# Kernel optimization log

Measured on AMD Instinct MI355X. Metric: run time of the kernel, lower is better.

## Reference

```python
import jax, jax.numpy as jnp
import numpy as np

N_NODES = 8192
N_EDGES = 262144
IN_DIM = 256
HID = 256
OUT_DIM = 64
PATH_DIM = 64
N_HEADS = 4


def setup_inputs() -> dict:
    key = jax.random.key(0)
    ks = jax.random.split(key, 16)
    s = 0.05
    x = jax.random.normal(ks[0], (N_NODES, IN_DIM), dtype=jnp.float32)
    edge_index = jax.random.randint(ks[1], (2, N_EDGES), 0, N_NODES, dtype=jnp.int32)
    return {
        "x": x,
        "edge_index": edge_index,
        # pathway encoder Linear(IN_DIM, PATH_DIM)
        "pe_w": jax.random.normal(ks[2], (IN_DIM, PATH_DIM), jnp.float32) * s,
        "pe_b": jax.random.normal(ks[3], (PATH_DIM,), jnp.float32) * s,
        # MultiheadAttention packed in-proj [3E, E] and out-proj [E, E]
        "in_proj_w": jax.random.normal(ks[4], (3 * PATH_DIM, PATH_DIM), jnp.float32) * s,
        "in_proj_b": jax.random.normal(ks[5], (3 * PATH_DIM,), jnp.float32) * s,
        "out_proj_w": jax.random.normal(ks[6], (PATH_DIM, PATH_DIM), jnp.float32) * s,
        "out_proj_b": jax.random.normal(ks[7], (PATH_DIM,), jnp.float32) * s,
        # GCN layer weights (in_dim, out_dim) + bias
        "w1": jax.random.normal(ks[8], (IN_DIM + PATH_DIM, HID), jnp.float32) * s,
        "b1": jax.random.normal(ks[9], (HID,), jnp.float32) * s,
        "w2": jax.random.normal(ks[10], (HID, HID), jnp.float32) * s,
        "b2": jax.random.normal(ks[11], (HID,), jnp.float32) * s,
        "w3": jax.random.normal(ks[12], (HID, OUT_DIM), jnp.float32) * s,
        "b3": jax.random.normal(ks[13], (OUT_DIM,), jnp.float32) * s,
    }


def mha_self(x, in_proj_w, in_proj_b, out_proj_w, out_proj_b):
    # unbatched nn.MultiheadAttention: x [N, E], Q=K=V=x
    N, E = x.shape
    dh = E // N_HEADS
    qkv = x @ in_proj_w.T + in_proj_b  # [N, 3E]
    q, k, v = jnp.split(qkv, 3, axis=-1)
    # [H, N, dh]
    q = q.reshape(N, N_HEADS, dh).transpose(1, 0, 2)
    k = k.reshape(N, N_HEADS, dh).transpose(1, 0, 2)
    v = v.reshape(N, N_HEADS, dh).transpose(1, 0, 2)
    scores = jnp.einsum('hnd,hmd->hnm', q, k) / jnp.sqrt(jnp.float32(dh))
    attn = jax.nn.softmax(scores, axis=-1)
    out = jnp.einsum('hnm,hmd->hnd', attn, v)  # [H, N, dh]
    out = out.transpose(1, 0, 2).reshape(N, E)
    return out @ out_proj_w.T + out_proj_b


def gcn_conv(h, edge_index, w, b, num_nodes):
    # PyG GCNConv: add self loops, symmetric normalization, linear, scatter-add, bias
    src = jnp.concatenate([edge_index[0], jnp.arange(num_nodes, dtype=edge_index.dtype)])
    dst = jnp.concatenate([edge_index[1], jnp.arange(num_nodes, dtype=edge_index.dtype)])
    deg = jax.ops.segment_sum(jnp.ones_like(dst, dtype=h.dtype), dst, num_segments=num_nodes)
    dinv = jnp.where(deg > 0, jax.lax.rsqrt(jnp.maximum(deg, 1e-12)), 0.0)
    hw = h @ w  # [N, out]
    norm = (dinv[src] * dinv[dst])[:, None]
    msg = hw[src] * norm
    out = jax.ops.segment_sum(msg, dst, num_segments=num_nodes)
    return out + b


def reference(x, edge_index, pe_w, pe_b, in_proj_w, in_proj_b, out_proj_w, out_proj_b,
              w1, b1, w2, b2, w3, b3):
    N = x.shape[0]
    pf = x @ pe_w + pe_b  # pathway encoder
    pa = mha_self(pf, in_proj_w, in_proj_b, out_proj_w, out_proj_b)
    h = jnp.concatenate([x, pa], axis=-1)  # [N, IN_DIM + PATH_DIM]
    h = jax.nn.relu(gcn_conv(h, edge_index, w1, b1, N))  # dropout is identity (eval)
    h = jax.nn.relu(gcn_conv(h, edge_index, w2, b2, N))
    h = gcn_conv(h, edge_index, w3, b3, N)
    return h
```

## Files before the change

### kernel.cpp

```cpp
#include <hip/hip_runtime.h>
#include <hip/hip_bf16.h>

#define N_NODES 8192
#define N_EDGES 262144
#define IN_DIM 256
#define HID 256
#define OUT_DIM 64
#define PATH_DIM 64
#define NHEADS 4
#define DH 16
#define KSPLIT 8
#define SPLIT_KEYS (N_NODES / KSPLIT)
#define NITER (SPLIT_KEYS / 64)

typedef __attribute__((ext_vector_type(8))) short bf16x8;
typedef __attribute__((ext_vector_type(4))) short bf16x4;
typedef __attribute__((ext_vector_type(4))) float f32x4;

__device__ __forceinline__ ushort f2bf(float f) {
  union { float f; unsigned int u; } c;
  c.f = f;
  unsigned int u = c.u;
  u += 0x7fffu + ((u >> 16) & 1u);
  return (ushort)(u >> 16);
}

__device__ __forceinline__ float fast_exp2(float x) {
  float r;
  asm("v_exp_f32 %0, %1" : "=v"(r) : "v"(x));
  return r;
}

__device__ __forceinline__ unsigned pack_bf16(float a, float b) {
  union { __hip_bfloat162 h; unsigned u; } c;
  c.h = __float22bfloat162_rn(make_float2(a, b));
  return c.u;
}

#if __has_builtin(__builtin_amdgcn_mfma_f32_16x16x16bf16_1k)
__device__ __forceinline__ f32x4 mfma16(bf16x4 a, bf16x4 b, f32x4 c) {
  return __builtin_amdgcn_mfma_f32_16x16x16bf16_1k(a, b, c, 0, 0, 0);
}
#else
__device__ __forceinline__ f32x4 mfma16(bf16x4 a, bf16x4 b, f32x4 c) {
  f32x4 d;
  asm volatile("v_mfma_f32_16x16x16_bf16 %0, %1, %2, %3\n\ts_nop 7\n\ts_nop 3"
               : "=v"(d) : "v"(a), "v"(b), "v"(c));
  return d;
}
#endif


__global__ __launch_bounds__(256) void init_graph(int* deg, int* cursor) {
  int i = blockIdx.x * 256 + threadIdx.x;
  if (i < N_NODES) { deg[i] = 1; cursor[i] = 0; }
}

__global__ __launch_bounds__(256) void count_deg(const int* __restrict__ dst,
                                                 int* __restrict__ deg) {
  int e = blockIdx.x * 256 + threadIdx.x;
  if (e < N_EDGES) atomicAdd(&deg[dst[e]], 1);
}

__global__ __launch_bounds__(256) void scan_rows(const int* __restrict__ deg,
                                                 int* __restrict__ row_off,
                                                 float* __restrict__ dinv) {
  __shared__ int part[256];
  int t = threadIdx.x;
  int base = t * 32;
  int local[32];
  int s = 0;
  #pragma unroll
  for (int i = 0; i < 32; ++i) {
    int c = deg[base + i] - 1;
    local[i] = s;
    s += c;
  }
  part[t] = s;
  __syncthreads();
  for (int d = 1; d < 256; d <<= 1) {
    int v = (t >= d) ? part[t - d] : 0;
    __syncthreads();
    part[t] += v;
    __syncthreads();
  }
  int prev = (t == 0) ? 0 : part[t - 1];
  #pragma unroll
  for (int i = 0; i < 32; ++i) {
    row_off[base + i] = prev + local[i];
    dinv[base + i] = rsqrtf((float)deg[base + i]);
  }
}

__global__ __launch_bounds__(256) void fill_csr(const int* __restrict__ src,
                                                const int* __restrict__ dst,
                                                const int* __restrict__ row_off,
                                                int* __restrict__ cursor,
                                                int* __restrict__ csr) {
  int e = blockIdx.x * 256 + threadIdx.x;
  if (e < N_EDGES) {
    int d = dst[e];
    int p = atomicAdd(&cursor[d], 1);
    csr[row_off[d] + p] = src[e];
  }
}


__global__ __launch_bounds__(256) void transpose_w(const float* __restrict__ W,
                                                   float* __restrict__ Wt,
                                                   int R, int C) {
  int i = blockIdx.x * 256 + threadIdx.x;
  if (i < R * C) {
    int r = i / C, c = i % C;
    Wt[c * R + r] = W[i];
  }
}

__global__ __launch_bounds__(256) void convert_qkv(const float* __restrict__ qkv,
                                                   ushort* __restrict__ Qbf,
                                                   ushort* __restrict__ Kbf,
                                                   ushort* __restrict__ Vtb) {
  const int tg = blockIdx.x * 256 + threadIdx.x;
  const int h = tg >> 13;
  const int n = tg & 8191;
  const float SC = 0.36067376022224085f;
  const float* base = qkv + (size_t)n * 192 + h * 16;
  ushort* qd = Qbf + ((size_t)h * 8192 + n) * 32;
  ushort* kd = Kbf + ((size_t)h * 8192 + n) * 32;
  ushort4 zz = make_ushort4(0, 0, 0, 0);
  #pragma unroll
  for (int i = 0; i < 16; i += 4) {
    float4 q4 = *reinterpret_cast<const float4*>(base + i);
    float4 k4 = *reinterpret_cast<const float4*>(base + 64 + i);
    float4 v4 = *reinterpret_cast<const float4*>(base + 128 + i);
    *reinterpret_cast<ushort4*>(qd + i) =
        make_ushort4(f2bf(q4.x * SC), f2bf(q4.y * SC), f2bf(q4.z * SC), f2bf(q4.w * SC));
    *reinterpret_cast<ushort4*>(kd + i) =
        make_ushort4(f2bf(k4.x), f2bf(k4.y), f2bf(k4.z), f2bf(k4.w));
    *reinterpret_cast<ushort4*>(qd + 16 + i) = zz;
    *reinterpret_cast<ushort4*>(kd + 16 + i) = zz;
    Vtb[((size_t)h * 16 + i + 0) * 8192 + n] = f2bf(v4.x);
    Vtb[((size_t)h * 16 + i + 1) * 8192 + n] = f2bf(v4.y);
    Vtb[((size_t)h * 16 + i + 2) * 8192 + n] = f2bf(v4.z);
    Vtb[((size_t)h * 16 + i + 3) * 8192 + n] = f2bf(v4.w);
  }
}


template <bool RELU, bool BIAS>
__global__ __launch_bounds__(256) void gemm_tile(const float* __restrict__ A1, int K1,
                                                 const float* __restrict__ A2, int K2,
                                                 const float* __restrict__ B,
                                                 const float* __restrict__ bias,
                                                 float* __restrict__ C, int N) {
  __shared__ __align__(16) float As[16][64];
  __shared__ __align__(16) float Bs[16][68];
  const int K = K1 + K2;
  const int bm = blockIdx.y * 64;
  const int bn = blockIdx.x * 64;
  const int t = threadIdx.x;
  const int tx = t & 15, ty = t >> 4;
  const int am = t >> 2;
  const int ak = (t & 3) << 2;
  const int bk = t >> 4;
  const int bn4 = (t & 15) << 2;
  float acc[4][4] = {};
  for (int k0 = 0; k0 < K; k0 += 16) {
    int kk = k0 + ak;
    int row = bm + am;
    float4 av;
    if (kk < K1)
      av = *reinterpret_cast<const float4*>(A1 + (size_t)row * K1 + kk);
    else
      av = *reinterpret_cast<const float4*>(A2 + (size_t)row * K2 + (kk - K1));
    As[ak + 0][am] = av.x;
    As[ak + 1][am] = av.y;
    As[ak + 2][am] = av.z;
    As[ak + 3][am] = av.w;
    float4 bv = *reinterpret_cast<const float4*>(B + (size_t)(k0 + bk) * N + bn + bn4);
    *reinterpret_cast<float4*>(&Bs[bk][bn4]) = bv;
    __syncthreads();
    #pragma unroll
    for (int k = 0; k < 16; ++k) {
      float4 a = *reinterpret_cast<const float4*>(&As[k][ty << 2]);
      float4 b = *reinterpret_cast<const float4*>(&Bs[k][tx << 2]);
      acc[0][0] += a.x * b.x; acc[0][1] += a.x * b.y; acc[0][2] += a.x * b.z; acc[0][3] += a.x * b.w;
      acc[1][0] += a.y * b.x; acc[1][1] += a.y * b.y; acc[1][2] += a.y * b.z; acc[1][3] += a.y * b.w;
      acc[2][0] += a.z * b.x; acc[2][1] += a.z * b.y; acc[2][2] += a.z * b.z; acc[2][3] += a.z * b.w;
      acc[3][0] += a.w * b.x; acc[3][1] += a.w * b.y; acc[3][2] += a.w * b.z; acc[3][3] += a.w * b.w;
    }
    __syncthreads();
  }
  #pragma unroll
  for (int i = 0; i < 4; ++i) {
    int row = bm + (ty << 2) + i;
    float4 o = make_float4(acc[i][0], acc[i][1], acc[i][2], acc[i][3]);
    if (BIAS) {
      float4 bv = *reinterpret_cast<const float4*>(bias + bn + (tx << 2));
      o.x += bv.x; o.y += bv.y; o.z += bv.z; o.w += bv.w;
    }
    if (RELU) {
      o.x = fmaxf(o.x, 0.f); o.y = fmaxf(o.y, 0.f);
      o.z = fmaxf(o.z, 0.f); o.w = fmaxf(o.w, 0.f);
    }
    *reinterpret_cast<float4*>(C + (size_t)row * N + bn + (tx << 2)) = o;
  }
}


__global__ __launch_bounds__(256) void attn_mfma5(const ushort* __restrict__ Qbf,
                                                  const ushort* __restrict__ Kbf,
                                                  const ushort* __restrict__ Vtb,
                                                  float* __restrict__ Opart,
                                                  float* __restrict__ Wpart) {
  const int h  = blockIdx.y;
  const int qb = blockIdx.x;
  const int kz = blockIdx.z;
  const int t  = threadIdx.x;
  const int wv = t >> 6;
  const int l  = t & 63;
  const int lg = l >> 4;
  const int lc = l & 15;

  __shared__ float red_o[3][64][17];
  __shared__ float red_w[3][64];

  bf16x8 qf[4];
  {
    const ushort* qbase = Qbf + ((size_t)h * 8192 + qb * 64) * 32;
    #pragma unroll
    for (int qt = 0; qt < 4; ++qt)
      qf[qt] = *reinterpret_cast<const bf16x8*>(qbase + (qt * 16 + lc) * 32 + lg * 8);
  }

  const ushort* kptr =
      Kbf + ((size_t)h * 8192 + kz * SPLIT_KEYS + wv * 16 + lc) * 32 + lg * 8;
  const ushort* vptr =
      Vtb + ((size_t)h * 16 + lc) * 8192 + kz * SPLIT_KEYS + wv * 16 + lg * 4;

  f32x4 oacc[4] = {{0.f, 0.f, 0.f, 0.f}, {0.f, 0.f, 0.f, 0.f},
                   {0.f, 0.f, 0.f, 0.f}, {0.f, 0.f, 0.f, 0.f}};
  float wsum[4] = {0.f, 0.f, 0.f, 0.f};

  bf16x8 kf = *reinterpret_cast<const bf16x8*>(kptr);
  bf16x4 vf = *reinterpret_cast<const bf16x4*>(vptr);

  for (int c = 0; c < NITER; ++c) {
    bf16x8 kf_n;
    bf16x4 vf_n;
    if (c + 1 < NITER) {
      kf_n = *reinterpret_cast<const bf16x8*>(kptr + (size_t)(c + 1) * 64 * 32);
      vf_n = *reinterpret_cast<const bf16x4*>(vptr + (size_t)(c + 1) * 64);
    }

    f32x4 s[4];
    #pragma unroll
    for (int qt = 0; qt < 4; ++qt) {
      f32x4 z = {0.f, 0.f, 0.f, 0.f};
      s[qt] = __builtin_amdgcn_mfma_f32_16x16x32_bf16(kf, qf[qt], z, 0, 0, 0);
    }

    #pragma unroll
    for (int qt = 0; qt < 4; ++qt) {
      float e0 = fast_exp2(s[qt][0]);
      float e1 = fast_exp2(s[qt][1]);
      float e2 = fast_exp2(s[qt][2]);
      float e3 = fast_exp2(s[qt][3]);
      wsum[qt] += (e0 + e1) + (e2 + e3);
      uint2 pk;
      pk.x = pack_bf16(e0, e1);
      pk.y = pack_bf16(e2, e3);
      bf16x4 pf;
      pf[0] = (short)(pk.x & 0xffff); pf[1] = (short)(pk.x >> 16);
      pf[2] = (short)(pk.y & 0xffff); pf[3] = (short)(pk.y >> 16);
      oacc[qt] = mfma16(pf, vf, oacc[qt]);
    }

    kf = kf_n;
    vf = vf_n;
  }

  #pragma unroll
  for (int qt = 0; qt < 4; ++qt) {
    float v = wsum[qt];
    v += __shfl_xor(v, 16);
    v += __shfl_xor(v, 32);
    wsum[qt] = v;
  }

  if (wv > 0) {
    #pragma unroll
    for (int qt = 0; qt < 4; ++qt) {
      #pragma unroll
      for (int r = 0; r < 4; ++r)
        red_o[wv - 1][qt * 16 + lg * 4 + r][lc] = oacc[qt][r];
      if (lg == 0) red_w[wv - 1][qt * 16 + lc] = wsum[qt];
    }
  }
  __syncthreads();

  if (wv == 0) {
    const size_t obase = ((size_t)(kz * NHEADS + h) * N_NODES + qb * 64);
    #pragma unroll
    for (int qt = 0; qt < 4; ++qt) {
      #pragma unroll
      for (int r = 0; r < 4; ++r) {
        const int q = qt * 16 + lg * 4 + r;
        float o = oacc[qt][r] + red_o[0][q][lc] + red_o[1][q][lc] + red_o[2][q][lc];
        Opart[(obase + q) * 16 + lc] = o;
      }
      if (lg == 0) {
        const int q = qt * 16 + lc;
        Wpart[obase + q] = wsum[qt] + red_w[0][q] + red_w[1][q] + red_w[2][q];
      }
    }
  }
}

__global__ __launch_bounds__(256) void attn_combine(const float* __restrict__ Opart,
                                                    const float* __restrict__ Wpart,
                                                    float* __restrict__ attn_out) {
  int i = blockIdx.x * 256 + threadIdx.x;
  int dq = i & 3;
  int hn = i >> 2;
  int h = hn >> 13;
  int n = hn & 8191;
  float4 acc = make_float4(0.f, 0.f, 0.f, 0.f);
  float ws = 0.f;
  #pragma unroll
  for (int s = 0; s < KSPLIT; ++s) {
    const size_t row = ((size_t)(s * NHEADS + h) * N_NODES + n);
    float4 v = *reinterpret_cast<const float4*>(Opart + row * 16 + dq * 4);
    acc.x += v.x; acc.y += v.y; acc.z += v.z; acc.w += v.w;
    ws += Wpart[row];
  }
  float inv = 1.f / ws;
  float4 o = make_float4(acc.x * inv, acc.y * inv, acc.z * inv, acc.w * inv);
  *reinterpret_cast<float4*>(attn_out + (size_t)n * 64 + h * 16 + dq * 4) = o;
}


template <bool RELU>
__global__ __launch_bounds__(256) void aggregate2(const float* __restrict__ hw,
                                                  const int* __restrict__ csr,
                                                  const int* __restrict__ row_off,
                                                  const int* __restrict__ deg,
                                                  const float* __restrict__ dinv,
                                                  const float* __restrict__ bias,
                                                  float* __restrict__ out) {
  __shared__ __align__(16) float part[2][256];
  const int t = threadIdx.x;
  const int rw = t >> 7;
  const int wh = (t >> 6) & 1;
  const int l = t & 63;
  const int r = blockIdx.x * 2 + rw;
  const float dr = dinv[r];
  const int off = row_off[r];
  const int cnt = deg[r] - 1;
  const int c = l << 2;

  float ax, ay, az, aw;
  if (wh == 0) {
    float4 a = *reinterpret_cast<const float4*>(hw + (size_t)r * 256 + c);
    ax = dr * a.x; ay = dr * a.y; az = dr * a.z; aw = dr * a.w;
  } else {
    ax = ay = az = aw = 0.f;
  }
  for (int e = wh; e < cnt; e += 2) {
    int s = csr[off + e];
    float wsc = dinv[s];
    float4 hv = *reinterpret_cast<const float4*>(hw + (size_t)s * 256 + c);
    ax += wsc * hv.x; ay += wsc * hv.y; az += wsc * hv.z; aw += wsc * hv.w;
  }
  if (wh == 1)
    *reinterpret_cast<float4*>(&part[rw][c]) = make_float4(ax, ay, az, aw);
  __syncthreads();
  if (wh == 0) {
    float4 p = *reinterpret_cast<const float4*>(&part[rw][c]);
    float4 bv = *reinterpret_cast<const float4*>(bias + c);
    float4 o;
    o.x = dr * (ax + p.x) + bv.x;
    o.y = dr * (ay + p.y) + bv.y;
    o.z = dr * (az + p.z) + bv.z;
    o.w = dr * (aw + p.w) + bv.w;
    if (RELU) {
      o.x = fmaxf(o.x, 0.f); o.y = fmaxf(o.y, 0.f);
      o.z = fmaxf(o.z, 0.f); o.w = fmaxf(o.w, 0.f);
    }
    *reinterpret_cast<float4*>(out + (size_t)r * 256 + c) = o;
  }
}

template <bool RELU>
__global__ __launch_bounds__(256) void aggregate64(const float* __restrict__ hw,
                                                   const int* __restrict__ csr,
                                                   const int* __restrict__ row_off,
                                                   const int* __restrict__ deg,
                                                   const float* __restrict__ dinv,
                                                   const float* __restrict__ bias,
                                                   float* __restrict__ out) {
  const int w = threadIdx.x >> 6, l = threadIdx.x & 63;
  const int r = blockIdx.x * 4 + w;
  const float dr = dinv[r];
  const int off = row_off[r];
  const int cnt = deg[r] - 1;
  float a = dr * hw[(size_t)r * 64 + l];
  for (int e = 0; e < cnt; ++e) {
    int s = csr[off + e];
    a += dinv[s] * hw[(size_t)s * 64 + l];
  }
  float o = dr * a + bias[l];
  if (RELU) o = fmaxf(o, 0.f);
  out[(size_t)r * 64 + l] = o;
}


extern "C" void kernel_launch(void* const* d_in, const int* in_sizes, int n_in,
                              void* d_out, int out_size, void* d_ws, size_t ws_size,
                              hipStream_t stream) {
  const float* x          = (const float*)d_in[0];
  const int*   ei         = (const int*)d_in[1];
  const float* pe_w       = (const float*)d_in[2];
  const float* pe_b       = (const float*)d_in[3];
  const float* in_proj_w  = (const float*)d_in[4];
  const float* in_proj_b  = (const float*)d_in[5];
  const float* out_proj_w = (const float*)d_in[6];
  const float* out_proj_b = (const float*)d_in[7];
  const float* w1         = (const float*)d_in[8];
  const float* b1         = (const float*)d_in[9];
  const float* w2         = (const float*)d_in[10];
  const float* b2         = (const float*)d_in[11];
  const float* w3         = (const float*)d_in[12];
  const float* b3         = (const float*)d_in[13];

  const int* esrc = ei;
  const int* edst = ei + N_EDGES;

  char* ws = (char*)d_ws;
  size_t o = 0;
  auto take = [&](size_t n) {
    char* p = ws + o;
    o += (n + 255) & ~(size_t)255;
    return p;
  };
  float* pf       = (float*)take((size_t)N_NODES * PATH_DIM * 4);
  float* qkv      = (float*)take((size_t)N_NODES * 3 * PATH_DIM * 4);
  float* attn_out = (float*)take((size_t)N_NODES * PATH_DIM * 4);
  float* pa       = (float*)take((size_t)N_NODES * PATH_DIM * 4);
  float* hw       = (float*)take((size_t)N_NODES * HID * 4);
  float* h1       = (float*)take((size_t)N_NODES * HID * 4);
  float* h2       = (float*)take((size_t)N_NODES * HID * 4);
  float* Wt_in    = (float*)take((size_t)3 * PATH_DIM * PATH_DIM * 4);
  float* Wt_out   = (float*)take((size_t)PATH_DIM * PATH_DIM * 4);
  float* dinv     = (float*)take((size_t)N_NODES * 4);
  int*   deg      = (int*)take((size_t)N_NODES * 4);
  int*   cursor   = (int*)take((size_t)N_NODES * 4);
  int*   row_off  = (int*)take((size_t)N_NODES * 4);
  int*   csr      = (int*)take((size_t)N_EDGES * 4);

  ushort* Qbf = (ushort*)h2;
  ushort* Kbf = Qbf + (size_t)NHEADS * N_NODES * 32;
  ushort* Vtb = Kbf + (size_t)NHEADS * N_NODES * 32;
  float* Opart = hw;
  float* Wpart = pa;

  init_graph<<<N_NODES / 256, 256, 0, stream>>>(deg, cursor);
  count_deg<<<N_EDGES / 256, 256, 0, stream>>>(edst, deg);
  scan_rows<<<1, 256, 0, stream>>>(deg, row_off, dinv);
  fill_csr<<<N_EDGES / 256, 256, 0, stream>>>(esrc, edst, row_off, cursor, csr);

  transpose_w<<<(192 * 64 + 255) / 256, 256, 0, stream>>>(in_proj_w, Wt_in, 192, 64);
  transpose_w<<<(64 * 64 + 255) / 256, 256, 0, stream>>>(out_proj_w, Wt_out, 64, 64);

  gemm_tile<false, true><<<dim3(1, 128), 256, 0, stream>>>(x, IN_DIM, nullptr, 0, pe_w, pe_b, pf, PATH_DIM);
  gemm_tile<false, true><<<dim3(3, 128), 256, 0, stream>>>(pf, PATH_DIM, nullptr, 0, Wt_in, in_proj_b, qkv, 3 * PATH_DIM);

  convert_qkv<<<(N_NODES * NHEADS) / 256, 256, 0, stream>>>(qkv, Qbf, Kbf, Vtb);
  attn_mfma5<<<dim3(128, 4, KSPLIT), 256, 0, stream>>>(Qbf, Kbf, Vtb, Opart, Wpart);
  attn_combine<<<(NHEADS * N_NODES * 4) / 256, 256, 0, stream>>>(Opart, Wpart, attn_out);

  gemm_tile<false, true><<<dim3(1, 128), 256, 0, stream>>>(attn_out, PATH_DIM, nullptr, 0, Wt_out, out_proj_b, pa, PATH_DIM);

  gemm_tile<false, false><<<dim3(4, 128), 256, 0, stream>>>(x, IN_DIM, pa, PATH_DIM, w1, nullptr, hw, HID);
  aggregate2<true><<<N_NODES / 2, 256, 0, stream>>>(hw, csr, row_off, deg, dinv, b1, h1);
  gemm_tile<false, false><<<dim3(4, 128), 256, 0, stream>>>(h1, HID, nullptr, 0, w2, nullptr, hw, HID);
  aggregate2<true><<<N_NODES / 2, 256, 0, stream>>>(hw, csr, row_off, deg, dinv, b2, h2);
  gemm_tile<false, false><<<dim3(1, 128), 256, 0, stream>>>(h2, HID, nullptr, 0, w3, nullptr, hw, OUT_DIM);
  aggregate64<false><<<N_NODES / 4, 256, 0, stream>>>(hw, csr, row_off, deg, dinv, b3, (float*)d_out);
}
```

Measured before the change: 296.9 us.

## Move GCN layers to bf16 MFMA GEMMs with split weights and bf16 activations

```diff
diff --git a/kernel.cpp b/kernel.cpp
--- a/kernel.cpp
+++ b/kernel.cpp
@@ -25,6 +25,12 @@
   return (ushort)(u >> 16);
 }
 
+__device__ __forceinline__ float bf2f(ushort u) {
+  union { float f; unsigned int u; } c;
+  c.u = ((unsigned int)u) << 16;
+  return c.f;
+}
+
 __device__ __forceinline__ float fast_exp2(float x) {
   float r;
   asm("v_exp_f32 %0, %1" : "=v"(r) : "v"(x));
@@ -114,6 +120,36 @@
     int r = i / C, c = i % C;
     Wt[c * R + r] = W[i];
   }
+}
+
+__global__ __launch_bounds__(256) void convert_wsplit(const float* __restrict__ W,
+                                                      ushort* __restrict__ Bthi,
+                                                      ushort* __restrict__ Btlo,
+                                                      int K, int N) {
+  int i = blockIdx.x * 256 + threadIdx.x;
+  if (i < K * N) {
+    int k = i / N, n = i % N;
+    float v = W[i];
+    ushort hi = f2bf(v);
+    ushort lo = f2bf(v - bf2f(hi));
+    Bthi[(size_t)n * K + k] = hi;
+    Btlo[(size_t)n * K + k] = lo;
+  }
+}
+
+__global__ __launch_bounds__(256) void convert_xpa(const float* __restrict__ x,
+                                                   const float* __restrict__ pa,
+                                                   ushort* __restrict__ Axpa) {
+  int i = blockIdx.x * 256 + threadIdx.x;
+  int n = i / 80;
+  int c = (i % 80) * 4;
+  float4 v;
+  if (c < 256)
+    v = *reinterpret_cast<const float4*>(x + (size_t)n * 256 + c);
+  else
+    v = *reinterpret_cast<const float4*>(pa + (size_t)n * 64 + (c - 256));
+  *reinterpret_cast<ushort4*>(Axpa + (size_t)n * 320 + c) =
+      make_ushort4(f2bf(v.x), f2bf(v.y), f2bf(v.z), f2bf(v.w));
 }
 
 __global__ __launch_bounds__(256) void convert_qkv(const float* __restrict__ qkv,
@@ -208,6 +244,44 @@
 }
 
 
+template <int K, int NT>
+__global__ __launch_bounds__(256) void gemm_mfma(const ushort* __restrict__ A,
+                                                 const ushort* __restrict__ Bthi,
+                                                 const ushort* __restrict__ Btlo,
+                                                 ushort* __restrict__ C) {
+  const int t = threadIdx.x;
+  const int wv = t >> 6;
+  const int l = t & 63;
+  const int lg = l >> 4;
+  const int lc = l & 15;
+  const int bm = blockIdx.y * 64;
+  const int n = blockIdx.x * 64 + wv * 16 + lc;
+
+  const ushort* ap = A + (size_t)(bm + lc) * K + lg * 8;
+  const ushort* bh = Bthi + (size_t)n * K + lg * 8;
+  const ushort* bl = Btlo + (size_t)n * K + lg * 8;
+
+  f32x4 acc[4] = {{0.f,0.f,0.f,0.f},{0.f,0.f,0.f,0.f},{0.f,0.f,0.f,0.f},{0.f,0.f,0.f,0.f}};
+  #pragma unroll 2
+  for (int k0 = 0; k0 < K; k0 += 32) {
+    bf16x8 vh = *reinterpret_cast<const bf16x8*>(bh + k0);
+    bf16x8 vl = *reinterpret_cast<const bf16x8*>(bl + k0);
+    #pragma unroll
+    for (int mt = 0; mt < 4; ++mt) {
+      bf16x8 af = *reinterpret_cast<const bf16x8*>(ap + (size_t)mt * 16 * K + k0);
+      acc[mt] = __builtin_amdgcn_mfma_f32_16x16x32_bf16(af, vh, acc[mt], 0, 0, 0);
+      acc[mt] = __builtin_amdgcn_mfma_f32_16x16x32_bf16(af, vl, acc[mt], 0, 0, 0);
+    }
+  }
+  #pragma unroll
+  for (int mt = 0; mt < 4; ++mt) {
+    #pragma unroll
+    for (int r = 0; r < 4; ++r)
+      C[(size_t)(bm + mt * 16 + lg * 4 + r) * NT + n] = f2bf(acc[mt][r]);
+  }
+}
+
+
 __global__ __launch_bounds__(256) void attn_mfma5(const ushort* __restrict__ Qbf,
                                                   const ushort* __restrict__ Kbf,
                                                   const ushort* __restrict__ Vtb,
@@ -267,13 +341,10 @@
       float e2 = fast_exp2(s[qt][2]);
       float e3 = fast_exp2(s[qt][3]);
       wsum[qt] += (e0 + e1) + (e2 + e3);
-      uint2 pk;
-      pk.x = pack_bf16(e0, e1);
-      pk.y = pack_bf16(e2, e3);
-      bf16x4 pf;
-      pf[0] = (short)(pk.x & 0xffff); pf[1] = (short)(pk.x >> 16);
-      pf[2] = (short)(pk.y & 0xffff); pf[3] = (short)(pk.y >> 16);
-      oacc[qt] = mfma16(pf, vf, oacc[qt]);
+      union { uint2 u; bf16x4 v; } pu;
+      pu.u.x = pack_bf16(e0, e1);
+      pu.u.y = pack_bf16(e2, e3);
+      oacc[qt] = mfma16(pu.v, vf, oacc[qt]);
     }
 
     kf = kf_n;
@@ -340,14 +411,15 @@
 }
 
 
-template <bool RELU>
-__global__ __launch_bounds__(256) void aggregate2(const float* __restrict__ hw,
-                                                  const int* __restrict__ csr,
-                                                  const int* __restrict__ row_off,
-                                                  const int* __restrict__ deg,
-                                                  const float* __restrict__ dinv,
-                                                  const float* __restrict__ bias,
-                                                  float* __restrict__ out) {
+template <bool RELU, bool OUTBF>
+__global__ __launch_bounds__(256) void aggregate_bf(const ushort* __restrict__ hwb,
+                                                    const int* __restrict__ csr,
+                                                    const int* __restrict__ row_off,
+                                                    const int* __restrict__ deg,
+                                                    const float* __restrict__ dinv,
+                                                    const float* __restrict__ bias,
+                                                    ushort* __restrict__ outb,
+                                                    float* __restrict__ outf) {
   __shared__ __align__(16) float part[2][256];
   const int t = threadIdx.x;
   const int rw = t >> 7;
@@ -359,59 +431,62 @@
   const int cnt = deg[r] - 1;
   const int c = l << 2;
 
-  float ax, ay, az, aw;
+  float a0, a1, a2, a3;
   if (wh == 0) {
-    float4 a = *reinterpret_cast<const float4*>(hw + (size_t)r * 256 + c);
-    ax = dr * a.x; ay = dr * a.y; az = dr * a.z; aw = dr * a.w;
+    ushort4 u = *reinterpret_cast<const ushort4*>(hwb + (size_t)r * 256 + c);
+    a0 = dr * bf2f(u.x); a1 = dr * bf2f(u.y); a2 = dr * bf2f(u.z); a3 = dr * bf2f(u.w);
   } else {
-    ax = ay = az = aw = 0.f;
+    a0 = a1 = a2 = a3 = 0.f;
   }
   for (int e = wh; e < cnt; e += 2) {
     int s = csr[off + e];
     float wsc = dinv[s];
-    float4 hv = *reinterpret_cast<const float4*>(hw + (size_t)s * 256 + c);
-    ax += wsc * hv.x; ay += wsc * hv.y; az += wsc * hv.z; aw += wsc * hv.w;
+    ushort4 u = *reinterpret_cast<const ushort4*>(hwb + (size_t)s * 256 + c);
+    a0 += wsc * bf2f(u.x); a1 += wsc * bf2f(u.y);
+    a2 += wsc * bf2f(u.z); a3 += wsc * bf2f(u.w);
   }
   if (wh == 1)
-    *reinterpret_cast<float4*>(&part[rw][c]) = make_float4(ax, ay, az, aw);
+    *reinterpret_cast<float4*>(&part[rw][c]) = make_float4(a0, a1, a2, a3);
   __syncthreads();
   if (wh == 0) {
     float4 p = *reinterpret_cast<const float4*>(&part[rw][c]);
     float4 bv = *reinterpret_cast<const float4*>(bias + c);
-    float4 o;
-    o.x = dr * (ax + p.x) + bv.x;
-    o.y = dr * (ay + p.y) + bv.y;
-    o.z = dr * (az + p.z) + bv.z;
-    o.w = dr * (aw + p.w) + bv.w;
+    float o0 = dr * (a0 + p.x) + bv.x;
+    float o1 = dr * (a1 + p.y) + bv.y;
+    float o2 = dr * (a2 + p.z) + bv.z;
+    float o3 = dr * (a3 + p.w) + bv.w;
     if (RELU) {
-      o.x = fmaxf(o.x, 0.f); o.y = fmaxf(o.y, 0.f);
-      o.z = fmaxf(o.z, 0.f); o.w = fmaxf(o.w, 0.f);
-    }
-    *reinterpret_cast<float4*>(out + (size_t)r * 256 + c) = o;
-  }
-}
-
-template <bool RELU>
-__global__ __launch_bounds__(256) void aggregate64(const float* __restrict__ hw,
-                                                   const int* __restrict__ csr,
-                                                   const int* __restrict__ row_off,
-                                                   const int* __restrict__ deg,
-                                                   const float* __restrict__ dinv,
-                                                   const float* __restrict__ bias,
-                                                   float* __restrict__ out) {
+      o0 = fmaxf(o0, 0.f); o1 = fmaxf(o1, 0.f);
+      o2 = fmaxf(o2, 0.f); o3 = fmaxf(o3, 0.f);
+    }
+    if (OUTBF) {
+      *reinterpret_cast<ushort4*>(outb + (size_t)r * 256 + c) =
+          make_ushort4(f2bf(o0), f2bf(o1), f2bf(o2), f2bf(o3));
+    } else {
+      *reinterpret_cast<float4*>(outf + (size_t)r * 256 + c) =
+          make_float4(o0, o1, o2, o3);
+    }
+  }
+}
+
+__global__ __launch_bounds__(256) void aggregate64_bf(const ushort* __restrict__ hwb,
+                                                      const int* __restrict__ csr,
+                                                      const int* __restrict__ row_off,
+                                                      const int* __restrict__ deg,
+                                                      const float* __restrict__ dinv,
+                                                      const float* __restrict__ bias,
+                                                      float* __restrict__ out) {
   const int w = threadIdx.x >> 6, l = threadIdx.x & 63;
   const int r = blockIdx.x * 4 + w;
   const float dr = dinv[r];
   const int off = row_off[r];
   const int cnt = deg[r] - 1;
-  float a = dr * hw[(size_t)r * 64 + l];
+  float a = dr * bf2f(hwb[(size_t)r * 64 + l]);
   for (int e = 0; e < cnt; ++e) {
     int s = csr[off + e];
-    a += dinv[s] * hw[(size_t)s * 64 + l];
-  }
-  float o = dr * a + bias[l];
-  if (RELU) o = fmaxf(o, 0.f);
-  out[(size_t)r * 64 + l] = o;
+    a += dinv[s] * bf2f(hwb[(size_t)s * 64 + l]);
+  }
+  out[(size_t)r * 64 + l] = dr * a + bias[l];
 }
 
 
@@ -447,9 +522,16 @@
   float* qkv      = (float*)take((size_t)N_NODES * 3 * PATH_DIM * 4);
   float* attn_out = (float*)take((size_t)N_NODES * PATH_DIM * 4);
   float* pa       = (float*)take((size_t)N_NODES * PATH_DIM * 4);
-  float* hw       = (float*)take((size_t)N_NODES * HID * 4);
-  float* h1       = (float*)take((size_t)N_NODES * HID * 4);
-  float* h2       = (float*)take((size_t)N_NODES * HID * 4);
+  char*  region1  = take(18874368);
+  ushort* Qbf     = (ushort*)take((size_t)NHEADS * N_NODES * 32 * 2);
+  ushort* Kbf     = (ushort*)take((size_t)NHEADS * N_NODES * 32 * 2);
+  ushort* Vtb     = (ushort*)take((size_t)NHEADS * DH * N_NODES * 2);
+  ushort* Bt1hi   = (ushort*)take((size_t)HID * 320 * 2);
+  ushort* Bt1lo   = (ushort*)take((size_t)HID * 320 * 2);
+  ushort* Bt2hi   = (ushort*)take((size_t)HID * HID * 2);
+  ushort* Bt2lo   = (ushort*)take((size_t)HID * HID * 2);
+  ushort* Bt3hi   = (ushort*)take((size_t)OUT_DIM * HID * 2);
+  ushort* Bt3lo   = (ushort*)take((size_t)OUT_DIM * HID * 2);
   float* Wt_in    = (float*)take((size_t)3 * PATH_DIM * PATH_DIM * 4);
   float* Wt_out   = (float*)take((size_t)PATH_DIM * PATH_DIM * 4);
   float* dinv     = (float*)take((size_t)N_NODES * 4);
@@ -458,11 +540,13 @@
   int*   row_off  = (int*)take((size_t)N_NODES * 4);
   int*   csr      = (int*)take((size_t)N_EDGES * 4);
 
-  ushort* Qbf = (ushort*)h2;
-  ushort* Kbf = Qbf + (size_t)NHEADS * N_NODES * 32;
-  ushort* Vtb = Kbf + (size_t)NHEADS * N_NODES * 32;
-  float* Opart = hw;
-  float* Wpart = pa;
+  float* Opart = (float*)region1;
+  float* Wpart = (float*)(region1 + 16777216);
+  ushort* Axpa  = (ushort*)region1;
+  ushort* hwbf  = Axpa + (size_t)N_NODES * 320;
+  ushort* h1bf  = hwbf + (size_t)N_NODES * 256;
+  ushort* h2bf  = h1bf + (size_t)N_NODES * 256;
+  ushort* hw64  = h2bf + (size_t)N_NODES * 256;
 
   init_graph<<<N_NODES / 256, 256, 0, stream>>>(deg, cursor);
   count_deg<<<N_EDGES / 256, 256, 0, stream>>>(edst, deg);
@@ -471,20 +555,22 @@
 
   transpose_w<<<(192 * 64 + 255) / 256, 256, 0, stream>>>(in_proj_w, Wt_in, 192, 64);
   transpose_w<<<(64 * 64 + 255) / 256, 256, 0, stream>>>(out_proj_w, Wt_out, 64, 64);
+  convert_wsplit<<<(320 * 256 + 255) / 256, 256, 0, stream>>>(w1, Bt1hi, Bt1lo, 320, HID);
+  convert_wsplit<<<(256 * 256 + 255) / 256, 256, 0, stream>>>(w2, Bt2hi, Bt2lo, HID, HID);
+  convert_wsplit<<<(256 * 64 + 255) / 256, 256, 0, stream>>>(w3, Bt3hi, Bt3lo, HID, OUT_DIM);
 
   gemm_tile<false, true><<<dim3(1, 128), 256, 0, stream>>>(x, IN_DIM, nullptr, 0, pe_w, pe_b, pf, PATH_DIM);
   gemm_tile<false, true><<<dim3(3, 128), 256, 0, stream>>>(pf, PATH_DIM, nullptr, 0, Wt_in, in_proj_b, qkv, 3 * PATH_DIM);
-
   convert_qkv<<<(N_NODES * NHEADS) / 256, 256, 0, stream>>>(qkv, Qbf, Kbf, Vtb);
   attn_mfma5<<<dim3(128, 4, KSPLIT), 256, 0, stream>>>(Qbf, Kbf, Vtb, Opart, Wpart);
   attn_combine<<<(NHEADS * N_NODES * 4) / 256, 256, 0, stream>>>(Opart, Wpart, attn_out);
-
   gemm_tile<false, true><<<dim3(1, 128), 256, 0, stream>>>(attn_out, PATH_DIM, nullptr, 0, Wt_out, out_proj_b, pa, PATH_DIM);
 
-  gemm_tile<false, false><<<dim3(4, 128), 256, 0, stream>>>(x, IN_DIM, pa, PATH_DIM, w1, nullptr, hw, HID);
-  aggregate2<true><<<N_NODES / 2, 256, 0, stream>>>(hw, csr, row_off, deg, dinv, b1, h1);
-  gemm_tile<false, false><<<dim3(4, 128), 256, 0, stream>>>(h1, HID, nullptr, 0, w2, nullptr, hw, HID);
-  aggregate2<true><<<N_NODES / 2, 256, 0, stream>>>(hw, csr, row_off, deg, dinv, b2, h2);
-  gemm_tile<false, false><<<dim3(1, 128), 256, 0, stream>>>(h2, HID, nullptr, 0, w3, nullptr, hw, OUT_DIM);
-  aggregate64<false><<<N_NODES / 4, 256, 0, stream>>>(hw, csr, row_off, deg, dinv, b3, (float*)d_out);
-}
+  convert_xpa<<<(N_NODES * 80) / 256, 256, 0, stream>>>(x, pa, Axpa);
+  gemm_mfma<320, 256><<<dim3(4, 128), 256, 0, stream>>>(Axpa, Bt1hi, Bt1lo, hwbf);
+  aggregate_bf<true, true><<<N_NODES / 2, 256, 0, stream>>>(hwbf, csr, row_off, deg, dinv, b1, h1bf, nullptr);
+  gemm_mfma<256, 256><<<dim3(4, 128), 256, 0, stream>>>(h1bf, Bt2hi, Bt2lo, hwbf);
+  aggregate_bf<true, true><<<N_NODES / 2, 256, 0, stream>>>(hwbf, csr, row_off, deg, dinv, b2, h2bf, nullptr);
+  gemm_mfma<256, 64><<<dim3(1, 128), 256, 0, stream>>>(h2bf, Bt3hi, Bt3lo, hw64);
+  aggregate64_bf<<<N_NODES / 4, 256, 0, stream>>>(hw64, csr, row_off, deg, dinv, b3, (float*)d_out);
+}
```

Result: faster. 275.1 us (-7.3%).
